# Optimization experiments

Measured on AMD Instinct MI355X. Metric: run time of the kernel, lower is better.

The kernel has to match this reference:

```python
import jax, jax.numpy as jnp
import numpy as np

N_NODES, D_IN, D_OUT, N_REL, N_EDGES = 100000, 128, 128, 8, 625000


def setup_inputs() -> dict:
    key = jax.random.key(0)
    ks = jax.random.split(key, 6)
    x = jax.random.normal(ks[0], (N_NODES, D_IN), dtype=jnp.float32)
    edge_index = jax.random.randint(ks[1], (2, N_EDGES), 0, N_NODES, dtype=jnp.int64)
    edge_type = jax.random.randint(ks[2], (N_EDGES,), 0, N_REL, dtype=jnp.int64)
    lim = (6.0 / (D_IN + D_OUT)) ** 0.5  # xavier_uniform
    rel_weight = jax.random.uniform(ks[3], (N_REL, D_IN, D_OUT), jnp.float32, -lim, lim)
    self_loop_weight = jax.random.uniform(ks[4], (D_IN, D_OUT), jnp.float32, -lim, lim)
    bias = jnp.zeros((D_OUT,), jnp.float32)
    return dict(x=x, edge_index=edge_index, edge_type=edge_type,
                rel_weight=rel_weight, self_loop_weight=self_loop_weight, bias=bias)


def reference(x, edge_index, edge_type, rel_weight, self_loop_weight, bias):
    N = x.shape[0]
    R = rel_weight.shape[0]
    src, dst = edge_index[0], edge_index[1]
    # Per-(relation, dst) in-degree == torch.bincount(dst) within each relation mask.
    seg = edge_type * N + dst  # combined (rel, dst) segment id
    deg = jax.ops.segment_sum(jnp.ones_like(src, dtype=x.dtype), seg, num_segments=R * N)
    deg = jnp.maximum(deg, 1.0)
    # Transform all node features by each relation weight once: [R, N, Do].
    xW = jnp.einsum('nd,rde->rne', x, rel_weight)
    # Gather per-edge messages already transformed by the edge's relation.
    messages = xW[edge_type, src] / deg[seg][:, None]  # [E, Do]
    out = x @ self_loop_weight + jax.ops.segment_sum(messages, dst, num_segments=N)
    return out + bias
```

## Files before the change

### kernel.cpp

```cpp
#include <hip/hip_runtime.h>

#define N_NODES 100000
#define DIM 128
#define N_REL 8
#define N_EDGES 625000
#define RN 800000
#define N_PADROWS 100032
#define SCAN_BLOCKS 98
#define SCAN_CHUNK 8192

__device__ __forceinline__ unsigned short f2bf(float f) {
    unsigned int u = __float_as_uint(f);
    u += 0x7fffu + ((u >> 16) & 1u);
    return (unsigned short)(u >> 16);
}

__device__ __forceinline__ float bf2f(unsigned short s) {
    return __uint_as_float(((unsigned int)s) << 16);
}

__global__ __launch_bounds__(256) void prep_kernel(const float* __restrict__ x,
                                                   const float* __restrict__ relw,
                                                   const float* __restrict__ selfw,
                                                   const int* __restrict__ dst,
                                                   const int* __restrict__ rel,
                                                   unsigned short* __restrict__ xb,
                                                   unsigned short* __restrict__ Wt,
                                                   int* __restrict__ degi,
                                                   int* __restrict__ rank) {
    int i = blockIdx.x * 256 + threadIdx.x;
    {
        float4 v = *(const float4*)(x + (size_t)i * 4);
        unsigned short t[4] = {f2bf(v.x), f2bf(v.y), f2bf(v.z), f2bf(v.w)};
        *(uint2*)(xb + (size_t)i * 4) = *(const uint2*)t;
    }
    if (i < 512) {
        uint4 z = {0, 0, 0, 0};
        *(uint4*)(xb + (size_t)N_NODES * DIM + i * 8) = z;
    }
    if (i < 147456) {
        int j = i & 7;
        int lane = (i >> 3) & 63;
        int t = (i >> 9) & 7;
        int ks = (i >> 12) & 3;
        int r = i >> 14;
        int m16 = lane & 15, quad = lane >> 4;
        int din = ks * 32 + quad * 8 + j;
        int dout = t * 16 + m16;
        float v = (r < 8) ? relw[(r << 14) + (din << 7) + dout] : selfw[(din << 7) + dout];
        Wt[i] = f2bf(v);
    }
    if (i < N_EDGES) {
        rank[i] = atomicAdd(&degi[rel[i] * N_NODES + dst[i]], 1);
    }
}

__global__ __launch_bounds__(256) void scan_kernel(const int* __restrict__ degi,
                                                   unsigned int* __restrict__ status,
                                                   int* __restrict__ offs) {
    __shared__ int lsum[256];
    __shared__ int lpfx;
    const int tid = threadIdx.x;
    const int b = blockIdx.x;
    const int base = b * SCAN_CHUNK + tid * 32;
    int v[32];
    int s = 0;
#pragma unroll
    for (int j = 0; j < 8; j++) {
        int idx = base + j * 4;
        int4 d = {0, 0, 0, 0};
        if (idx + 3 < RN) d = *(const int4*)(degi + idx);
        else {
            if (idx < RN) d.x = degi[idx];
            if (idx + 1 < RN) d.y = degi[idx + 1];
            if (idx + 2 < RN) d.z = degi[idx + 2];
        }
        v[j * 4] = d.x; v[j * 4 + 1] = d.y; v[j * 4 + 2] = d.z; v[j * 4 + 3] = d.w;
        s += d.x + d.y + d.z + d.w;
    }
    lsum[tid] = s;
    __syncthreads();
    for (int off = 1; off < 256; off <<= 1) {
        int p = (tid >= off) ? lsum[tid - off] : 0;
        __syncthreads();
        lsum[tid] += p;
        __syncthreads();
    }
    int thrbase = lsum[tid] - s;
    int total = lsum[255];

    if (b == 0) {
        if (tid == 0) {
            atomicExch(&status[0], 0x80000000u | (unsigned)total);
            lpfx = 0;
        }
    } else {
        if (tid == 0) atomicExch(&status[b], 0x40000000u | (unsigned)total);
        if (tid < 64) {
            int sum = 0;
            int j = b - 1;
            while (true) {
                int idx = j - tid;
                unsigned st = (idx >= 0) ? atomicAdd(&status[idx], 0u) : 0x80000000u;
                unsigned long long pball = __ballot(st & 0x80000000u);
                unsigned long long zball = __ballot(st == 0u);
                int fp = pball ? (__ffsll(pball) - 1) : 64;
                unsigned long long below = (fp >= 64) ? ~0ull : ((1ull << fp) - 1ull);
                if (zball & below) continue;
                int lim = (fp < 64) ? fp : 63;
                int val = (tid <= lim) ? (int)(st & 0x3fffffffu) : 0;
                for (int o = 32; o > 0; o >>= 1) val += __shfl_down(val, o);
                sum += __shfl(val, 0);
                if (fp < 64) break;
                j -= 64;
            }
            if (tid == 0) {
                atomicExch(&status[b], 0x80000000u | (unsigned)(sum + total));
                lpfx = sum;
            }
        }
    }
    __syncthreads();
    int run = lpfx + thrbase;
#pragma unroll
    for (int j = 0; j < 32; j++) {
        int idx = base + j;
        if (idx < RN) {
            offs[idx] = run;
            if (idx == RN - 1) offs[RN] = run + v[j];
            run += v[j];
        }
    }
}

__global__ __launch_bounds__(256) void fill_kernel(const int* __restrict__ src,
                                                   const int* __restrict__ dst,
                                                   const int* __restrict__ rel,
                                                   const int* __restrict__ rank,
                                                   const int* __restrict__ offs,
                                                   unsigned int* __restrict__ ebuf) {
    int e = blockIdx.x * 256 + threadIdx.x;
    if (e < N_EDGES) {
        int d = dst[e];
        int key = rel[e] * N_NODES + d;
        int pos = offs[key] + rank[e];
        ebuf[pos] = (unsigned int)src[e] | ((unsigned int)(d & 15) << 17);
    }
}

typedef __attribute__((ext_vector_type(8))) short frag8;
typedef __attribute__((ext_vector_type(4))) float f32x4;

__global__ __launch_bounds__(256, 4) void fused_kernel(const unsigned short* __restrict__ xb,
                                                       const unsigned short* __restrict__ Wt,
                                                       const int* __restrict__ offs2,
                                                       const unsigned int* __restrict__ ebuf,
                                                       const float* __restrict__ bias,
                                                       float* __restrict__ out) {
    __shared__ __align__(16) unsigned char ldsraw[16384];

    const int tid = threadIdx.x;
    const int wave = tid >> 6, lane = tid & 63;
    const int g = wave >> 1, h = wave & 1;
    const int m16 = lane & 15, quad = lane >> 4;
    const int dbase = blockIdx.x * 32 + g * 16;
    unsigned char* slab = ldsraw + wave * 4096;

    int cidx = dbase + lane;
    if (cidx > N_NODES) cidx = N_NODES;
    const int* obase = offs2 + (size_t)h * 4 * N_NODES + cidx;

    int obc = obase[0];
    int obn = obase[N_NODES];

    f32x4 acc[8];
#pragma unroll
    for (int t = 0; t < 8; t++) acc[t] = (f32x4){0.f, 0.f, 0.f, 0.f};

    int s0 = __builtin_amdgcn_readlane(obc, 0);
    int count = __builtin_amdgcn_readlane(obc, 16) - s0;
    unsigned int ewc = 0;
    if (lane < count) ewc = ebuf[s0 + lane];

    if (h == 0) {
        const unsigned short* ap = xb + (size_t)(dbase + m16) * DIM;
#pragma unroll
        for (int ks = 0; ks < 4; ks++) {
            frag8 a = *(const frag8*)(ap + ks * 32 + quad * 8);
            const frag8* bp = (const frag8*)Wt + ((8 * 4 + ks) * 8) * 64 + lane;
#pragma unroll
            for (int t = 0; t < 8; t++)
                acc[t] = __builtin_amdgcn_mfma_f32_16x16x32_bf16(a, bp[t * 64], acc[t], 0, 0, 0);
        }
    }

    unsigned int u0[8], v0[8];
    if (count > 0) {
        int cl = count; if (cl > 64) cl = 64;
#pragma unroll
        for (int k = 0; k < 8; k++) {
            int li = k; if (li >= cl) li = cl - 1;
            u0[k] = (unsigned int)__builtin_amdgcn_readlane((int)ewc, li);
            v0[k] = *((const unsigned int*)xb + (size_t)(u0[k] & 0x1ffffu) * 64 + lane);
        }
    }

#pragma unroll 1
    for (int r = 0; r < 4; r++) {
        int s0n = __builtin_amdgcn_readlane(obn, 0);
        int cntn = __builtin_amdgcn_readlane(obn, 16) - s0n;
        unsigned int ewn = 0;
        if (r < 3 && lane < cntn) ewn = ebuf[s0n + lane];
        int obn2 = (r < 2) ? obase[(r + 2) * N_NODES] : 0;

        {
            uint4 z = {0, 0, 0, 0};
            *(uint4*)(slab + lane * 16) = z;
            *(uint4*)(slab + 1024 + lane * 16) = z;
            *(uint4*)(slab + 2048 + lane * 16) = z;
            *(uint4*)(slab + 3072 + lane * 16) = z;
        }

        if (count > 0) {
            float ax = 0.f, ay = 0.f;
            int cur = -1, cnt = 0;
#pragma unroll 1
            for (int b0 = 0; b0 < count; b0 += 64) {
                int cl = count - b0; if (cl > 64) cl = 64;
                unsigned int ew = ewc;
                if (b0 > 0) {
                    ew = 0;
                    if (b0 + lane < count) ew = ebuf[s0 + b0 + lane];
#pragma unroll
                    for (int k = 0; k < 8; k++) {
                        int li = k; if (li >= cl) li = cl - 1;
                        u0[k] = (unsigned int)__builtin_amdgcn_readlane((int)ew, li);
                        v0[k] = *((const unsigned int*)xb + (size_t)(u0[k] & 0x1ffffu) * 64 + lane);
                    }
                }
#pragma unroll 1
                for (int i = 0; i < cl; i += 8) {
                    unsigned int u1[8], v1[8];
                    if (i + 8 < cl) {
#pragma unroll
                        for (int k = 0; k < 8; k++) {
                            int li = i + 8 + k; if (li >= cl) li = cl - 1;
                            u1[k] = (unsigned int)__builtin_amdgcn_readlane((int)ew, li);
                            v1[k] = *((const unsigned int*)xb + (size_t)(u1[k] & 0x1ffffu) * 64 + lane);
                        }
                    }
                    int kk = cl - i; if (kk > 8) kk = 8;
#pragma unroll
                    for (int k = 0; k < 8; k++) {
                        if (k < kk) {
                            int dl = (int)((u0[k] >> 17) & 15u);
                            if (dl != cur) {
                                if (cnt > 0) {
                                    float inv = 1.0f / (float)cnt;
                                    unsigned int p = (unsigned int)f2bf(ax * inv) |
                                                     ((unsigned int)f2bf(ay * inv) << 16);
                                    int bb = (lane >> 2) ^ cur;
                                    *(unsigned int*)(slab + cur * 256 + bb * 16 + (lane & 3) * 4) = p;
                                }
                                cur = dl; ax = 0.f; ay = 0.f; cnt = 0;
                            }
                            ax += bf2f((unsigned short)(v0[k] & 0xffffu));
                            ay += bf2f((unsigned short)(v0[k] >> 16));
                            cnt++;
                        }
                    }
                    if (i + 8 < cl) {
#pragma unroll
                        for (int k = 0; k < 8; k++) { u0[k] = u1[k]; v0[k] = v1[k]; }
                    }
                }
            }
            {
                float inv = 1.0f / (float)cnt;
                unsigned int p = (unsigned int)f2bf(ax * inv) |
                                 ((unsigned int)f2bf(ay * inv) << 16);
                int bb = (lane >> 2) ^ cur;
                *(unsigned int*)(slab + cur * 256 + bb * 16 + (lane & 3) * 4) = p;
            }
        }

        if (r < 3 && cntn > 0) {
            int cl = cntn; if (cl > 64) cl = 64;
#pragma unroll
            for (int k = 0; k < 8; k++) {
                int li = k; if (li >= cl) li = cl - 1;
                u0[k] = (unsigned int)__builtin_amdgcn_readlane((int)ewn, li);
                v0[k] = *((const unsigned int*)xb + (size_t)(u0[k] & 0x1ffffu) * 64 + lane);
            }
        }

#pragma unroll
        for (int ks = 0; ks < 4; ks++) {
            int bb = (4 * ks + quad) ^ m16;
            frag8 a = *(const frag8*)(slab + m16 * 256 + bb * 16);
            const frag8* bp = (const frag8*)Wt + (((h * 4 + r) * 4 + ks) * 8) * 64 + lane;
#pragma unroll
            for (int t = 0; t < 8; t++)
                acc[t] = __builtin_amdgcn_mfma_f32_16x16x32_bf16(a, bp[t * 64], acc[t], 0, 0, 0);
        }

        s0 = s0n; count = cntn; ewc = ewn; obn = obn2;
    }

    __syncthreads();
    unsigned char* mbuf = ldsraw + g * 8192;
    if (h == 1) {
#pragma unroll
        for (int t = 0; t < 8; t++)
            *(f32x4*)(mbuf + (t * 64 + lane) * 16) = acc[t];
    }
    __syncthreads();
    if (h == 0) {
#pragma unroll
        for (int t = 0; t < 8; t++) {
            f32x4 m = *(f32x4*)(mbuf + (t * 64 + lane) * 16);
            acc[t] += m;
        }

        float* S = (float*)mbuf;
#pragma unroll
        for (int hh = 0; hh < 2; hh++) {
#pragma unroll
            for (int tt = 0; tt < 4; tt++) {
                int t = hh * 4 + tt;
                float bc = bias[t * 16 + m16];
#pragma unroll
                for (int i = 0; i < 4; i++)
                    S[(quad * 4 + i) * 68 + tt * 16 + m16] = acc[t][i] + bc;
            }
#pragma unroll
            for (int c = 0; c < 4; c++) {
                int row16 = c * 4 + quad;
                int gr = dbase + row16;
                if (gr < N_NODES)
                    *(float4*)(out + (size_t)gr * DIM + hh * 64 + m16 * 4) =
                        *(float4*)(S + row16 * 68 + m16 * 4);
            }
        }
    }
}

extern "C" void kernel_launch(void* const* d_in, const int* in_sizes, int n_in,
                              void* d_out, int out_size, void* d_ws, size_t ws_size,
                              hipStream_t stream) {
    const float* x = (const float*)d_in[0];
    const int* edge_index = (const int*)d_in[1];
    const int* edge_type = (const int*)d_in[2];
    const float* relw = (const float*)d_in[3];
    const float* selfw = (const float*)d_in[4];
    const float* bias = (const float*)d_in[5];
    float* out = (float*)d_out;
    (void)in_sizes; (void)n_in; (void)out_size; (void)ws_size;

    char* ws = (char*)d_ws;
    size_t off = 0;
    unsigned short* xb = (unsigned short*)(ws + off); off += (size_t)N_PADROWS * DIM * 2;
    unsigned short* Wt = (unsigned short*)(ws + off); off += (size_t)9 * DIM * DIM * 2;
    int* offs2 = (int*)(ws + off); off += (size_t)(RN + 4) * 4;
    unsigned int* ebuf = (unsigned int*)(ws + off); off += (size_t)N_EDGES * 4;

    int* degi = (int*)d_out;
    unsigned int* status = (unsigned int*)(degi + RN);
    int* rank = (int*)(status + SCAN_BLOCKS + 2);

    const int* src = edge_index;
    const int* dst = edge_index + N_EDGES;

    hipMemsetAsync(degi, 0, (size_t)RN * 4 + (SCAN_BLOCKS + 2) * 4, stream);
    prep_kernel<<<12500, 256, 0, stream>>>(x, relw, selfw, dst, edge_type, xb, Wt, degi, rank);
    scan_kernel<<<SCAN_BLOCKS, 256, 0, stream>>>(degi, status, offs2);
    fill_kernel<<<(N_EDGES + 255) / 256, 256, 0, stream>>>(src, dst, edge_type, rank, offs2, ebuf);
    fused_kernel<<<N_PADROWS / 32, 256, 0, stream>>>(xb, Wt, offs2, ebuf, bias, out);
}
```

Baseline: 255.0 us.

## Gather neighbor rows via global_load_lds DMA into LDS slots instead of registers

Edge-row gathers now use global_load_lds to copy each source row straight into per-wave LDS slots, 16 rows per batch, rather than prefetching 8 rows into VGPRs. The edge lists for all four relations are loaded up front, and the next relation's first batch is issued before the MFMA step. Reciprocal uses rcpf and bf16 unpacking is simplified. LDS per block doubles to 32KB, which may cut occupancy. Each batch also waits on vmcnt(0), so gather latency is less overlapped within a relation.

```diff
diff --git a/kernel.cpp b/kernel.cpp
--- a/kernel.cpp
+++ b/kernel.cpp
@@ -151,36 +151,53 @@
 typedef __attribute__((ext_vector_type(8))) short frag8;
 typedef __attribute__((ext_vector_type(4))) float f32x4;
 
+__device__ __forceinline__ void row_dma(const unsigned int* g, unsigned int* l) {
+    __builtin_amdgcn_global_load_lds(g, l, 4, 0, 0);
+}
+
 __global__ __launch_bounds__(256, 4) void fused_kernel(const unsigned short* __restrict__ xb,
                                                        const unsigned short* __restrict__ Wt,
                                                        const int* __restrict__ offs2,
                                                        const unsigned int* __restrict__ ebuf,
                                                        const float* __restrict__ bias,
                                                        float* __restrict__ out) {
-    __shared__ __align__(16) unsigned char ldsraw[16384];
+    __shared__ __align__(16) unsigned char ldsraw[4 * 8192];
 
     const int tid = threadIdx.x;
     const int wave = tid >> 6, lane = tid & 63;
     const int g = wave >> 1, h = wave & 1;
     const int m16 = lane & 15, quad = lane >> 4;
     const int dbase = blockIdx.x * 32 + g * 16;
-    unsigned char* slab = ldsraw + wave * 4096;
+    unsigned char* slab = ldsraw + wave * 8192;
+    unsigned int* slots32 = (unsigned int*)(slab + 4096);
+    const unsigned int* xb32 = (const unsigned int*)xb;
 
     int cidx = dbase + lane;
     if (cidx > N_NODES) cidx = N_NODES;
     const int* obase = offs2 + (size_t)h * 4 * N_NODES + cidx;
 
-    int obc = obase[0];
-    int obn = obase[N_NODES];
+    int obA = obase[0];
+    int obB = obase[N_NODES];
+    int obC = obase[2 * N_NODES];
+    int obD = obase[3 * N_NODES];
+    int sA = __builtin_amdgcn_readlane(obA, 0);
+    int cA = __builtin_amdgcn_readlane(obA, 16) - sA;
+    int sB = __builtin_amdgcn_readlane(obB, 0);
+    int cB = __builtin_amdgcn_readlane(obB, 16) - sB;
+    int sC = __builtin_amdgcn_readlane(obC, 0);
+    int cC = __builtin_amdgcn_readlane(obC, 16) - sC;
+    int sD = __builtin_amdgcn_readlane(obD, 0);
+    int cD = __builtin_amdgcn_readlane(obD, 16) - sD;
+
+    unsigned int ewA = 0, ewB = 0, ewC = 0, ewD = 0;
+    if (lane < cA) ewA = ebuf[sA + lane];
+    if (lane < cB) ewB = ebuf[sB + lane];
+    if (lane < cC) ewC = ebuf[sC + lane];
+    if (lane < cD) ewD = ebuf[sD + lane];
 
     f32x4 acc[8];
 #pragma unroll
     for (int t = 0; t < 8; t++) acc[t] = (f32x4){0.f, 0.f, 0.f, 0.f};
-
-    int s0 = __builtin_amdgcn_readlane(obc, 0);
-    int count = __builtin_amdgcn_readlane(obc, 16) - s0;
-    unsigned int ewc = 0;
-    if (lane < count) ewc = ebuf[s0 + lane];
 
     if (h == 0) {
         const unsigned short* ap = xb + (size_t)(dbase + m16) * DIM;
@@ -194,25 +211,19 @@
         }
     }
 
-    unsigned int u0[8], v0[8];
-    if (count > 0) {
-        int cl = count; if (cl > 64) cl = 64;
-#pragma unroll
-        for (int k = 0; k < 8; k++) {
-            int li = k; if (li >= cl) li = cl - 1;
-            u0[k] = (unsigned int)__builtin_amdgcn_readlane((int)ewc, li);
-            v0[k] = *((const unsigned int*)xb + (size_t)(u0[k] & 0x1ffffu) * 64 + lane);
+    {
+        int cl0 = cA < 16 ? cA : 16;
+#pragma unroll
+        for (int k = 0; k < 16; k++) {
+            if (k < cl0) {
+                int row = (int)(((unsigned)__builtin_amdgcn_readlane((int)ewA, k)) & 0x1ffffu);
+                row_dma(xb32 + (size_t)row * 64 + lane, slots32 + k * 64);
+            }
         }
     }
 
 #pragma unroll 1
     for (int r = 0; r < 4; r++) {
-        int s0n = __builtin_amdgcn_readlane(obn, 0);
-        int cntn = __builtin_amdgcn_readlane(obn, 16) - s0n;
-        unsigned int ewn = 0;
-        if (r < 3 && lane < cntn) ewn = ebuf[s0n + lane];
-        int obn2 = (r < 2) ? obase[(r + 2) * N_NODES] : 0;
-
         {
             uint4 z = {0, 0, 0, 0};
             *(uint4*)(slab + lane * 16) = z;
@@ -221,42 +232,47 @@
             *(uint4*)(slab + 3072 + lane * 16) = z;
         }
 
-        if (count > 0) {
+        if (cA > 0) {
             float ax = 0.f, ay = 0.f;
             int cur = -1, cnt = 0;
 #pragma unroll 1
-            for (int b0 = 0; b0 < count; b0 += 64) {
-                int cl = count - b0; if (cl > 64) cl = 64;
-                unsigned int ew = ewc;
+            for (int b0 = 0; b0 < cA; b0 += 64) {
+                int cl = cA - b0; if (cl > 64) cl = 64;
+                unsigned int ew = ewA;
                 if (b0 > 0) {
                     ew = 0;
-                    if (b0 + lane < count) ew = ebuf[s0 + b0 + lane];
-#pragma unroll
-                    for (int k = 0; k < 8; k++) {
-                        int li = k; if (li >= cl) li = cl - 1;
-                        u0[k] = (unsigned int)__builtin_amdgcn_readlane((int)ew, li);
-                        v0[k] = *((const unsigned int*)xb + (size_t)(u0[k] & 0x1ffffu) * 64 + lane);
-                    }
+                    if (b0 + lane < cA) ew = ebuf[sA + b0 + lane];
                 }
 #pragma unroll 1
-                for (int i = 0; i < cl; i += 8) {
-                    unsigned int u1[8], v1[8];
-                    if (i + 8 < cl) {
-#pragma unroll
-                        for (int k = 0; k < 8; k++) {
-                            int li = i + 8 + k; if (li >= cl) li = cl - 1;
-                            u1[k] = (unsigned int)__builtin_amdgcn_readlane((int)ew, li);
-                            v1[k] = *((const unsigned int*)xb + (size_t)(u1[k] & 0x1ffffu) * 64 + lane);
+                for (int i = 0; i < cl; i += 16) {
+                    if (b0 + i > 0) {
+                        asm volatile("s_waitcnt lgkmcnt(0)" ::: "memory");
+#pragma unroll
+                        for (int k = 0; k < 16; k++) {
+                            if (i + k < cl) {
+                                int row = (int)(((unsigned)__builtin_amdgcn_readlane((int)ew, i + k)) & 0x1ffffu);
+                                row_dma(xb32 + (size_t)row * 64 + lane, slots32 + k * 64);
+                            }
                         }
                     }
-                    int kk = cl - i; if (kk > 8) kk = 8;
-#pragma unroll
-                    for (int k = 0; k < 8; k++) {
+                    asm volatile("s_waitcnt vmcnt(0)" ::: "memory");
+                    __builtin_amdgcn_sched_barrier(0);
+
+                    int kk = cl - i; if (kk > 16) kk = 16;
+                    unsigned int vv[16];
+#pragma unroll
+                    for (int k = 0; k < 16; k++) {
+                        int sk = k; if (sk >= kk) sk = kk - 1;
+                        vv[k] = slots32[sk * 64 + lane];
+                    }
+#pragma unroll
+                    for (int k = 0; k < 16; k++) {
                         if (k < kk) {
-                            int dl = (int)((u0[k] >> 17) & 15u);
+                            unsigned int uu = (unsigned)__builtin_amdgcn_readlane((int)ew, i + k);
+                            int dl = (int)((uu >> 17) & 15u);
                             if (dl != cur) {
                                 if (cnt > 0) {
-                                    float inv = 1.0f / (float)cnt;
+                                    float inv = __builtin_amdgcn_rcpf((float)cnt);
                                     unsigned int p = (unsigned int)f2bf(ax * inv) |
                                                      ((unsigned int)f2bf(ay * inv) << 16);
                                     int bb = (lane >> 2) ^ cur;
@@ -264,19 +280,15 @@
                                 }
                                 cur = dl; ax = 0.f; ay = 0.f; cnt = 0;
                             }
-                            ax += bf2f((unsigned short)(v0[k] & 0xffffu));
-                            ay += bf2f((unsigned short)(v0[k] >> 16));
+                            ax += __uint_as_float(vv[k] << 16);
+                            ay += __uint_as_float(vv[k] & 0xffff0000u);
                             cnt++;
                         }
                     }
-                    if (i + 8 < cl) {
-#pragma unroll
-                        for (int k = 0; k < 8; k++) { u0[k] = u1[k]; v0[k] = v1[k]; }
-                    }
                 }
             }
             {
-                float inv = 1.0f / (float)cnt;
+                float inv = __builtin_amdgcn_rcpf((float)cnt);
                 unsigned int p = (unsigned int)f2bf(ax * inv) |
                                  ((unsigned int)f2bf(ay * inv) << 16);
                 int bb = (lane >> 2) ^ cur;
@@ -284,13 +296,15 @@
             }
         }
 
-        if (r < 3 && cntn > 0) {
-            int cl = cntn; if (cl > 64) cl = 64;
-#pragma unroll
-            for (int k = 0; k < 8; k++) {
-                int li = k; if (li >= cl) li = cl - 1;
-                u0[k] = (unsigned int)__builtin_amdgcn_readlane((int)ewn, li);
-                v0[k] = *((const unsigned int*)xb + (size_t)(u0[k] & 0x1ffffu) * 64 + lane);
+        asm volatile("s_waitcnt lgkmcnt(0)" ::: "memory");
+        if (r < 3) {
+            int cln = cB < 16 ? cB : 16;
+#pragma unroll
+            for (int k = 0; k < 16; k++) {
+                if (k < cln) {
+                    int row = (int)(((unsigned)__builtin_amdgcn_readlane((int)ewB, k)) & 0x1ffffu);
+                    row_dma(xb32 + (size_t)row * 64 + lane, slots32 + k * 64);
+                }
             }
         }
 
@@ -304,11 +318,13 @@
                 acc[t] = __builtin_amdgcn_mfma_f32_16x16x32_bf16(a, bp[t * 64], acc[t], 0, 0, 0);
         }
 
-        s0 = s0n; count = cntn; ewc = ewn; obn = obn2;
+        sA = sB; cA = cB; ewA = ewB;
+        sB = sC; cB = cC; ewB = ewC;
+        sC = sD; cC = cD; ewC = ewD;
     }
 
     __syncthreads();
-    unsigned char* mbuf = ldsraw + g * 8192;
+    unsigned char* mbuf = ldsraw + g * 16384;
     if (h == 1) {
 #pragma unroll
         for (int t = 0; t < 8; t++)
```

Measured after the change: 268.0 us. 5.1% more time.
